# Kernel optimization log

Measured on AMD Instinct MI355X. Metric: run time of the kernel, lower is better.

The kernel has to match this reference:

```python
import jax, jax.numpy as jnp
import numpy as np

TAU = 1.5
K = 4
EPS = 1e-5
GN_GROUPS = 8

def conv2d(x, w, pad, rhs_dilation=(1, 1)):
    return jax.lax.conv_general_dilated(
        x, w, window_strides=(1, 1),
        padding=[(pad, pad), (pad, pad)],
        rhs_dilation=rhs_dilation,
        dimension_numbers=("NCHW", "OIHW", "NCHW"))

def setup_inputs() -> dict:
    key = jax.random.key(0)
    ks = jax.random.split(key, 16)
    s = 0.05  # weight scale to keep activations sane
    B, C, H, W = 16, 128, 64, 64
    O, HID, CG, SE = 128, 32, 16, 16
    d = {}
    d["x"] = jax.random.normal(ks[0], (B, C, H, W), jnp.float32)
    d["base_weight"] = jax.random.normal(ks[1], (O, C, 3, 3), jnp.float32) * s
    d["delta_weight"] = jax.random.normal(ks[2], (K, O, C, 3, 3), jnp.float32) * s
    d["kernel_scale"] = jnp.ones((K, O, 1, 1, 1), jnp.float32)
    d["gc_w1"] = jax.random.normal(ks[3], (HID, C), jnp.float32) * s
    d["gc_w2"] = jax.random.normal(ks[4], (C, HID), jnp.float32) * s
    d["rc_w"] = jax.random.normal(ks[5], (HID, C, 3, 3), jnp.float32) * s
    d["bn_gamma"] = jnp.ones((HID,), jnp.float32)
    d["bn_beta"] = jnp.zeros((HID,), jnp.float32)
    d["bn_mean"] = jnp.zeros((HID,), jnp.float32)
    d["bn_var"] = jnp.ones((HID,), jnp.float32)
    d["rg_w"] = jax.random.normal(ks[6], (HID, C), jnp.float32) * s
    d["gate_w"] = jax.random.normal(ks[7], (K * O, HID), jnp.float32) * s
    d["gate_b"] = jnp.zeros((K * O,), jnp.float32)
    d["cg_w1"] = jax.random.normal(ks[8], (CG, C), jnp.float32) * s
    d["cg_b1"] = jnp.zeros((CG,), jnp.float32)
    d["cg_w2"] = jax.random.normal(ks[9], (C, CG), jnp.float32) * s
    d["cg_b2"] = jnp.zeros((C,), jnp.float32)
    d["sg_w"] = jax.random.normal(ks[10], (1, 2, 7, 7), jnp.float32) * s
    d["gn_gamma"] = jnp.ones((O,), jnp.float32)
    d["gn_beta"] = jnp.zeros((O,), jnp.float32)
    d["se_w1"] = jax.random.normal(ks[11], (SE, O), jnp.float32) * s
    d["se_b1"] = jnp.zeros((SE,), jnp.float32)
    d["se_w2"] = jax.random.normal(ks[12], (O, SE), jnp.float32) * s
    d["se_b2"] = jnp.zeros((O,), jnp.float32)
    d["identity_scale"] = jnp.float32(0.0)
    d["bias"] = jnp.zeros((O,), jnp.float32)
    return d

def reference(x, base_weight, delta_weight, kernel_scale, gc_w1, gc_w2, rc_w,
              bn_gamma, bn_beta, bn_mean, bn_var, rg_w, gate_w, gate_b,
              cg_w1, cg_b1, cg_w2, cg_b2, sg_w, gn_gamma, gn_beta,
              se_w1, se_b1, se_w2, se_b2, identity_scale, bias):
    identity = x
    B, C, H, W = x.shape
    O = base_weight.shape[0]

    # global context gate (squeeze-excite style)
    p = x.mean((2, 3))                                    # [B,C]
    g = jax.nn.sigmoid(jax.nn.silu(p @ gc_w1.T) @ gc_w2.T)
    x = x * g[:, :, None, None]

    # channel gate
    pc = x.mean((2, 3))
    c_attn = jax.nn.sigmoid(jax.nn.silu(pc @ cg_w1.T + cg_b1) @ cg_w2.T + cg_b2)
    # spatial gate
    s_in = jnp.concatenate([x.mean(1, keepdims=True), x.max(1, keepdims=True)], axis=1)
    s_attn = jax.nn.sigmoid(conv2d(s_in, sg_w, pad=3))
    x = x * c_attn[:, :, None, None] * s_attn

    # router: dilated conv + BN(eval) + SiLU, plus global branch
    lf = conv2d(x, rc_w, pad=2, rhs_dilation=(2, 2))
    lf = (lf - bn_mean[None, :, None, None]) * jax.lax.rsqrt(bn_var + EPS)[None, :, None, None]
    lf = lf * bn_gamma[None, :, None, None] + bn_beta[None, :, None, None]
    lf = jax.nn.silu(lf)
    gf = jax.nn.silu(x.mean((2, 3)) @ rg_w.T)             # [B,HID]
    lf = lf + gf[:, :, None, None]
    alpha = jnp.einsum("bhij,oh->boij", lf, gate_w) + gate_b[None, :, None, None]
    alpha = alpha.reshape(B, K, O, H, W)
    alpha = jax.nn.softmax(alpha / TAU, axis=1)

    # unfold (k=3, stride=1, pad=1, dilation=1) -> H_out=H, W_out=W
    xp = jnp.pad(x, ((0, 0), (0, 0), (1, 1), (1, 1)))
    patches = jnp.stack([xp[:, :, i:i + H, j:j + W]
                         for i in range(3) for j in range(3)], axis=2)  # [B,C,9,H,W]
    L = H * W
    xu = patches.reshape(B, C * 9, L).transpose(0, 2, 1)  # [B,L,C*9]

    base = base_weight.reshape(O, -1)
    delta = (delta_weight * kernel_scale).reshape(K, O, -1)
    # same-size bilinear resize of alpha is the identity
    alpha_map = alpha.reshape(B, K, O, L)

    static = jnp.einsum("blf,of->bol", xu, base)          # [B,O,L]
    res = jnp.einsum("blf,kof->bkol", xu, delta)          # [B,K,O,L]
    final = static + (res * alpha_map).sum(1)
    out = final.reshape(B, O, H, W)

    # GroupNorm
    go = out.reshape(B, GN_GROUPS, O // GN_GROUPS, H, W)
    mu = go.mean((2, 3, 4), keepdims=True)
    var = go.var((2, 3, 4), keepdims=True)
    out = ((go - mu) * jax.lax.rsqrt(var + EPS)).reshape(B, O, H, W)
    out = out * gn_gamma[None, :, None, None] + gn_beta[None, :, None, None]

    # output SE
    ps = out.mean((2, 3))
    se = jax.nn.sigmoid(jax.nn.silu(ps @ se_w1.T + se_b1) @ se_w2.T + se_b2)
    out = out * se[:, :, None, None]

    out = out + jnp.tanh(identity_scale) * identity
    out = out + bias[None, :, None, None]
    return out
```

## Files before the change

kernel.cpp:

```cpp
#include <hip/hip_runtime.h>
#include <hip/hip_bf16.h>
#include <math.h>

typedef __bf16 bf16_t;
typedef __bf16 bf16x8 __attribute__((ext_vector_type(8)));
typedef __bf16 bf16x4 __attribute__((ext_vector_type(4)));
typedef float  f32x4  __attribute__((ext_vector_type(4)));

#define EPSF 1e-5f
#define TAUF 1.5f

__device__ __forceinline__ float sigmoidf_(float x){ return 1.f/(1.f+__expf(-x)); }
__device__ __forceinline__ float siluf_(float x){ return x*sigmoidf_(x); }

__device__ __forceinline__ void gload_lds16(const void* g, void* l){
  __builtin_amdgcn_global_load_lds((const __attribute__((address_space(1))) unsigned int*)g,
                                   (__attribute__((address_space(3))) unsigned int*)l, 16, 0, 0);
}

__global__ void k_prep(const float* __restrict__ base_w, const float* __restrict__ delta_w,
                       const float* __restrict__ kscale, const float* __restrict__ rc_w,
                       bf16_t* __restrict__ WCQ, bf16_t* __restrict__ RCWQ,
                       bf16_t* __restrict__ x2q,
                       const float* __restrict__ x, float* __restrict__ p){
  int bx = blockIdx.x;
  if (bx >= 2704){
    int bc = bx - 2704; const float* xr = x + (size_t)bc*4096;
    float s = 0.f;
    for (int i = threadIdx.x; i < 4096; i += 256) s += xr[i];
    __shared__ float sb[4];
    for (int off=32; off; off>>=1) s += __shfl_down(s, off);
    if ((threadIdx.x & 63)==0) sb[threadIdx.x>>6] = s;
    __syncthreads();
    if (threadIdx.x==0) p[bc] = (sb[0]+sb[1]+sb[2]+sb[3]) * (1.f/4096.f);
    return;
  }
  if (bx >= 2448){
    int pp = bx - 2448;
    size_t base = (size_t)pp*68*68*8;
    float4 z = {0.f,0.f,0.f,0.f};
    for (int i = threadIdx.x; i < 272; i += 256){
      int r = i/68; int wp = i - r*68;
      int hp = (r&1) + (r>>1)*66;
      *(float4*)(x2q + base + ((size_t)hp*68 + wp)*8) = z;
    }
    {
      int i = threadIdx.x;
      int hp = 2 + (i>>2);
      int wp = (i&1) + (i&2)*33;
      *(float4*)(x2q + base + ((size_t)hp*68 + wp)*8) = z;
    }
    return;
  }
  int i = bx*256 + threadIdx.x;
  if (i < 589824){
    int c8 = i&7; int o16 = (i>>3)&15; int q = (i>>7)&3; int s = (i>>9)&3;
    int h2 = (i>>11)&3; int r = i>>13; int t = r%9; int ob = r/9;
    int o = ob*16 + o16; int c = h2*32 + q*8 + c8;
    float v = base_w[(o*128+c)*9 + t] + delta_w[(((s*128)+o)*128 + c)*9 + t]*kscale[s*128+o];
    WCQ[i] = (bf16_t)v;
  } else if (i < 589824 + 36864){
    int j = i - 589824;
    int c8 = j&7; int h16 = (j>>3)&15; int q = (j>>7)&3; int n2 = (j>>9)&1;
    int r = j>>10; int t = r%9; int h2 = r/9;
    int hid = n2*16 + h16; int c = h2*32 + q*8 + c8;
    RCWQ[j] = (bf16_t)rc_w[(hid*128+c)*9 + t];
  }
}

__global__ void k_small1(const float* __restrict__ p, const float* __restrict__ gc_w1,
                         const float* __restrict__ gc_w2, const float* __restrict__ cg_w1,
                         const float* __restrict__ cg_b1, const float* __restrict__ cg_w2,
                         const float* __restrict__ cg_b2,
                         float* __restrict__ gbuf, float* __restrict__ gate){
  int b = blockIdx.x; int t = threadIdx.x;
  __shared__ float ps[128], h1[32], pc[128], c1[16];
  ps[t] = p[b*128+t];
  __syncthreads();
  if (t < 32){ float a=0.f; for(int c=0;c<128;c++) a += ps[c]*gc_w1[t*128+c]; h1[t]=siluf_(a); }
  __syncthreads();
  float a=0.f; for(int j=0;j<32;j++) a += h1[j]*gc_w2[t*32+j];
  float g = sigmoidf_(a);
  gbuf[b*128+t] = g; pc[t] = ps[t]*g;
  __syncthreads();
  if (t < 16){ float a2=cg_b1[t]; for(int c=0;c<128;c++) a2 += pc[c]*cg_w1[t*128+c]; c1[t]=siluf_(a2); }
  __syncthreads();
  float a3=cg_b2[t]; for(int j=0;j<16;j++) a3 += c1[j]*cg_w2[t*16+j];
  gate[b*128+t] = g * sigmoidf_(a3);
}

__global__ void k_spatial(const float* __restrict__ x, const float* __restrict__ gbuf,
                          float* __restrict__ sin_){
  int bi = blockIdx.x; int b = bi>>6; int h = bi&63;
  int wv = threadIdx.x>>6, w = threadIdx.x&63;
  __shared__ float psum[4][64], pmax[4][64];
  float sm=0.f, mx=-1e30f;
  const float* xb = x + (((size_t)b*128 + wv*32)*64 + h)*64 + w;
  const float* gb = gbuf + b*128 + wv*32;
  #pragma unroll 4
  for (int c=0;c<32;c++){
    float v = xb[(size_t)c*4096] * gb[c];
    sm += v; mx = fmaxf(mx, v);
  }
  psum[wv][w]=sm; pmax[wv][w]=mx;
  __syncthreads();
  if (threadIdx.x < 64){
    float s = psum[0][w]+psum[1][w]+psum[2][w]+psum[3][w];
    float m = fmaxf(fmaxf(pmax[0][w],pmax[1][w]),fmaxf(pmax[2][w],pmax[3][w]));
    sin_[b*8192 + h*64 + w]        = s*(1.f/128.f);
    sin_[b*8192 + 4096 + h*64 + w] = m;
  }
}

__global__ void __launch_bounds__(256) k_x2(
    const float* __restrict__ x, const float* __restrict__ gate,
    const float* __restrict__ sin_, const float* __restrict__ sg_w,
    bf16_t* __restrict__ x2q, float* __restrict__ pc2){
  int bi = blockIdx.x; int b = bi>>6; int h = bi&63;
  __shared__ float tile[128*65];
  __shared__ float sh_sin[980];
  __shared__ float sh_sgw[98];
  __shared__ float satt_row[64];
  int tid = threadIdx.x, wv = tid>>6, lane = tid&63;
  for (int i=tid;i<980;i+=256){
    int c2 = i/490; int rr = i - c2*490; int r = rr/70; int k = rr - r*70;
    int hh = h + r - 3; int ww = k - 3;
    float v = 0.f;
    if (hh>=0 && hh<64 && ww>=0 && ww<64) v = sin_[b*8192 + c2*4096 + hh*64 + ww];
    sh_sin[i] = v;
  }
  if (tid < 98) sh_sgw[tid] = sg_w[tid];
  __syncthreads();
  if (tid < 64){
    float a = 0.f;
    #pragma unroll
    for (int c2=0;c2<2;c2++)
      #pragma unroll
      for (int r=0;r<7;r++)
        #pragma unroll
        for (int j=0;j<7;j++)
          a += sh_sin[c2*490 + r*70 + tid + j] * sh_sgw[c2*49 + r*7 + j];
    satt_row[tid] = sigmoidf_(a);
  }
  __syncthreads();
  float sa = satt_row[lane];
  const float* xb = x + (((size_t)b*128 + wv*32)*64 + h)*64 + lane;
  const float* gb = gate + b*128 + wv*32;
  #pragma unroll 8
  for (int i=0;i<32;i++)
    tile[(wv*32+i)*65 + lane] = xb[(size_t)i*4096] * gb[i] * sa;
  __syncthreads();
  for (int it=0; it<4; it++){
    int idx = it*256 + tid;
    int cq = idx>>6; int w = idx&63;
    int c0 = cq*8;
    bf16x8 v;
    #pragma unroll
    for (int e=0;e<8;e++) v[e] = (bf16_t)tile[(c0+e)*65 + w];
    *(bf16x8*)(x2q + (((((size_t)b*4 + (cq>>2))*4 + (cq&3))*68 + (h+2))*68 + (w+2))*8) = v;
  }
  if (tid < 128){
    const float* row = &tile[tid*65];
    float s = 0.f;
    #pragma unroll 8
    for (int w=0;w<64;w++) s += row[w];
    atomicAdd(&pc2[b*128+tid], s);
  }
}

__global__ void __launch_bounds__(256) k_router(
    const bf16_t* __restrict__ x2q, const bf16_t* __restrict__ RCWQ,
    const float* __restrict__ bn_gamma, const float* __restrict__ bn_beta,
    const float* __restrict__ bn_mean, const float* __restrict__ bn_var,
    const float* __restrict__ pc2, const float* __restrict__ rg_w,
    bf16_t* __restrict__ lfb){
  __shared__ __align__(16) char smem[44544];
  __shared__ float sgf[32];
  __shared__ float spart[256];
  int tid = threadIdx.x;
  int wv = tid>>6, lane = tid&63, m16 = lane&15, q = lane>>4;
  int rb = blockIdx.x & 31, b = blockIdx.x >> 5;
  int r0 = rb*2;
  int rloc = wv&1;
  int ws0 = (wv>>1)*2;

  {
    int hid = tid&31, seg = tid>>5;
    float a=0.f;
    #pragma unroll
    for (int j=0;j<16;j++) a += pc2[b*128 + seg*16 + j]*rg_w[hid*128 + seg*16 + j];
    spart[tid] = a;
  }

  f32x4 acc[2][2] = {};

  #pragma unroll 1
  for (int h2=0; h2<4; h2++){
    const char* asrc = (const char*)(x2q + ((((size_t)(b*4+h2)*4 + wv)*68 + r0)*68)*8);
    #pragma unroll
    for (int j=0;j<7;j++){
      if (j*64 + lane < 408)
        gload_lds16(asrc + j*1024 + lane*16, (char*)smem + wv*6528 + j*1024);
    }
    const char* wsrc = (const char*)(RCWQ + (size_t)h2*9216) + wv*4608;
    #pragma unroll
    for (int j=0;j<5;j++){
      if (j*64 + lane < 288)
        gload_lds16(wsrc + j*1024 + lane*16, (char*)smem + 26112 + wv*4608 + j*1024);
    }
    __syncthreads();
    if (h2==0 && tid < 32){
      float s = 0.f;
      #pragma unroll
      for (int k=0;k<8;k++) s += spart[k*32+tid];
      sgf[tid] = siluf_(s*(1.f/4096.f));
    }
    #pragma unroll
    for (int t=0; t<9; t++){
      int di = t/3, dj = t - di*3;
      bf16x8 aw0 = *(const bf16x8*)((const char*)smem + 26112 + (t*2+0)*1024 + q*256 + m16*16);
      bf16x8 aw1 = *(const bf16x8*)((const char*)smem + 26112 + (t*2+1)*1024 + q*256 + m16*16);
      #pragma unroll
      for (int mt=0; mt<2; mt++){
        int wseg = ws0 + mt;
        bf16x8 bs = *(const bf16x8*)((const char*)smem + q*6528 +
                     ((rloc + 2*di)*68 + wseg*16 + m16 + 2*dj)*16);
        acc[0][mt] = __builtin_amdgcn_mfma_f32_16x16x32_bf16(aw0, bs, acc[0][mt], 0,0,0);
        acc[1][mt] = __builtin_amdgcn_mfma_f32_16x16x32_bf16(aw1, bs, acc[1][mt], 0,0,0);
      }
    }
    __syncthreads();
  }

  #pragma unroll
  for (int n2=0;n2<2;n2++){
    float aa[4], bb[4];
    #pragma unroll
    for (int i=0;i<4;i++){
      int hid = n2*16 + q*4 + i;
      float a = bn_gamma[hid]*rsqrtf(bn_var[hid]+EPSF);
      aa[i] = a;
      bb[i] = bn_beta[hid] - bn_mean[hid]*a;
    }
    #pragma unroll
    for (int mt=0;mt<2;mt++){
      bf16x4 yv;
      #pragma unroll
      for (int i=0;i<4;i++){
        int hid = n2*16 + q*4 + i;
        yv[i] = (bf16_t)(siluf_(aa[i]*acc[n2][mt][i] + bb[i]) + sgf[hid]);
      }
      size_t pos = (size_t)b*4096 + (r0+rloc)*64 + (ws0+mt)*16 + m16;
      *(bf16x4*)(lfb + pos*32 + n2*16 + q*4) = yv;
    }
  }
}

__global__ void __launch_bounds__(512, 2) k_main(
    const bf16_t* __restrict__ x2q, const bf16_t* __restrict__ WCQ,
    const bf16_t* __restrict__ lfb, const float* __restrict__ gate_w,
    const float* __restrict__ gate_b, bf16_t* __restrict__ outp,
    float* __restrict__ csum, float* __restrict__ cssq){
  __shared__ __align__(16) char smem[161920];
  float* sred = (float*)(smem + 160896);

  int tid = threadIdx.x;
  int wv = tid>>6, lane = tid&63, m16 = lane&15, q = lane>>4;
  int hf = wv>>2, w4 = wv&3;
  int bx = blockIdx.x;
  int ob2 = bx >> 7; int rem = bx & 127; int b = rem >> 3; int hb = rem & 7;
  int h0 = hb*8;
  int obase = (ob2*2 + hf)*16;

  auto STAGE_A = [&](int h2, int bsel){
    int quad = wv>>1, rh = wv&1;
    const char* asrc = (const char*)(x2q + ((((size_t)(b*4+h2)*4 + quad)*68 + (h0+1+rh*5))*68)*8);
    char* adst = (char*)smem + bsel*43584 + quad*10896 + rh*5440;
    #pragma unroll
    for (int j=0;j<6;j++){
      if (j*64 + lane < 340)
        gload_lds16(asrc + (j*64+lane)*16, adst + j*1024);
    }
  };
  auto STAGE_B = [&](int h2){
    int obh = ob2*2 + hf;
    const char* wsrc = (const char*)WCQ + (size_t)(obh*9*4 + h2)*4096;
    char* bdst = (char*)smem + 87168 + hf*36864 + w4*9216;
    #pragma unroll
    for (int j=0;j<9;j++){
      int cc = w4*576 + j*64 + lane;
      int tap = cc>>8, r = cc&255;
      gload_lds16(wsrc + tap*16384 + r*16, bdst + j*1024);
    }
  };

  f32x4 acc[8][4] = {};

  int baseA[8];
  #pragma unroll
  for (int mi=0;mi<8;mi++){
    int row = w4*2 + (mi>>2); int wseg = mi&3;
    baseA[mi] = q*10896 + (row*68 + wseg*16 + m16 + 1)*16;
  }
  int baseB = q*256 + m16*16;

  STAGE_A(0, 0);
  STAGE_B(0);

  #pragma unroll 1
  for (int h2=0; h2<4; h2++){
    if (h2 < 3){
      STAGE_A(h2+1, (h2+1)&1);
      asm volatile("s_waitcnt vmcnt(6)" ::: "memory");
    } else {
      asm volatile("s_waitcnt vmcnt(0)" ::: "memory");
    }
    __builtin_amdgcn_s_barrier();

    const char* Ab = (const char*)smem + (h2&1)*43584;
    const char* Bb = (const char*)smem + 87168 + hf*36864;
    #pragma unroll
    for (int t=0; t<9; t++){
      int di = t/3, dj = t - di*3;
      int toff = (di*68 + dj)*16;
      bf16x8 av[8], bv[4];
      #pragma unroll
      for (int mi=0;mi<8;mi++) av[mi] = *(const bf16x8*)(Ab + baseA[mi] + toff);
      #pragma unroll
      for (int s=0;s<4;s++)  bv[s] = *(const bf16x8*)(Bb + t*4096 + s*1024 + baseB);
      #pragma unroll
      for (int s=0;s<4;s++){
        #pragma unroll
        for (int mi=0;mi<8;mi++)
          acc[mi][s] = __builtin_amdgcn_mfma_f32_16x16x32_bf16(av[mi], bv[s], acc[mi][s], 0,0,0);
      }
    }
    __builtin_amdgcn_s_barrier();
    if (h2 < 3) STAGE_B(h2+1);
  }

  const char* lfsrc = (const char*)(lfb + ((size_t)b*4096 + h0*64)*32);
  #pragma unroll
  for (int j=0;j<4;j++)
    gload_lds16(lfsrc + j*8192 + wv*1024 + lane*16, (char*)smem + j*8192 + wv*1024);
  bf16_t* shGW = (bf16_t*)(smem + 32768);
  for (int idx = tid; idx < 4096; idx += 512){
    int hf2 = idx>>11; int n = (idx>>5)&63; int j2 = idx&31;
    shGW[idx] = (bf16_t)gate_w[((n>>4)*128 + (ob2*2+hf2)*16 + (n&15))*32 + j2];
  }
  __syncthreads();

  bf16x8 bg[4];
  #pragma unroll
  for (int kk=0;kk<4;kk++)
    bg[kk] = *(const bf16x8*)((const char*)shGW + hf*4096 + (kk*16+m16)*64 + q*16);
  float gb[4];
  #pragma unroll
  for (int kk=0;kk<4;kk++) gb[kk] = gate_b[kk*128 + obase + m16];

  const float itau = 1.f/TAUF;
  float s1 = 0.f, s2 = 0.f;
  size_t orow = ((size_t)(b*128 + obase + m16))*4096 + h0*64;
  #pragma unroll
  for (int mi=0; mi<8; mi++){
    bf16x8 avL = *(const bf16x8*)((const char*)smem + (w4*128 + mi*16 + m16)*64 + q*16);
    f32x4 zero = {};
    f32x4 lg[4];
    #pragma unroll
    for (int kk=0;kk<4;kk++)
      lg[kk] = __builtin_amdgcn_mfma_f32_16x16x32_bf16(avL, bg[kk], zero, 0,0,0);
    bf16x4 yv;
    #pragma unroll
    for (int r=0;r<4;r++){
      float l0 = (lg[0][r]+gb[0])*itau, l1 = (lg[1][r]+gb[1])*itau;
      float l2 = (lg[2][r]+gb[2])*itau, l3 = (lg[3][r]+gb[3])*itau;
      float mx = fmaxf(fmaxf(l0,l1),fmaxf(l2,l3));
      float e0=__expf(l0-mx), e1=__expf(l1-mx), e2=__expf(l2-mx), e3=__expf(l3-mx);
      float inv = 1.f/(e0+e1+e2+e3);
      float y = (e0*acc[mi][0][r] + e1*acc[mi][1][r]
               + e2*acc[mi][2][r] + e3*acc[mi][3][r])*inv;
      s1 += y; s2 += y*y;
      yv[r] = (bf16_t)y;
    }
    *(bf16x4*)(outp + orow + w4*128 + mi*16 + q*4) = yv;
  }

  s1 += __shfl_down(s1, 32); s1 += __shfl_down(s1, 16);
  s2 += __shfl_down(s2, 32); s2 += __shfl_down(s2, 16);
  if (lane < 16){ sred[wv*16 + lane] = s1; sred[128 + wv*16 + lane] = s2; }
  __syncthreads();
  if (tid < 32){
    int hf2 = tid>>4, o = tid&15;
    float a = 0.f, c = 0.f;
    #pragma unroll
    for (int k=0;k<4;k++){
      a += sred[(hf2*4+k)*16 + o];
      c += sred[128 + (hf2*4+k)*16 + o];
    }
    atomicAdd(&csum[b*128 + (ob2*2+hf2)*16 + o], a);
    atomicAdd(&cssq[b*128 + (ob2*2+hf2)*16 + o], c);
  }
}

__global__ void k_small3(const float* __restrict__ csum, const float* __restrict__ cssq,
                         const float* __restrict__ gn_gamma, const float* __restrict__ gn_beta,
                         const float* __restrict__ se_w1, const float* __restrict__ se_b1,
                         const float* __restrict__ se_w2, const float* __restrict__ se_b2,
                         float* __restrict__ sca, float* __restrict__ shb){
  int b = blockIdx.x; int o = threadIdx.x;
  __shared__ float s1[128], s2[128], gmu[8], grs[8], psl[128], t1[16];
  s1[o] = csum[b*128+o]; s2[o] = cssq[b*128+o];
  __syncthreads();
  if (o<8){
    float a=0.f,a2=0.f; for(int j=0;j<16;j++){ a+=s1[o*16+j]; a2+=s2[o*16+j]; }
    float mu = a*(1.f/65536.f); float var = a2*(1.f/65536.f) - mu*mu;
    gmu[o]=mu; grs[o]=rsqrtf(var+EPSF);
  }
  __syncthreads();
  int g = o>>4;
  psl[o] = (s1[o]*(1.f/4096.f) - gmu[g])*grs[g]*gn_gamma[o] + gn_beta[o];
  __syncthreads();
  if (o<16){ float a = se_b1[o]; for(int c=0;c<128;c++) a += psl[c]*se_w1[o*128+c]; t1[o]=siluf_(a); }
  __syncthreads();
  float a = se_b2[o]; for(int j=0;j<16;j++) a += t1[j]*se_w2[o*16+j];
  float sev = sigmoidf_(a);
  sca[b*128+o] = grs[g]*gn_gamma[o]*sev;
  shb[b*128+o] = (gn_beta[o] - gmu[g]*grs[g]*gn_gamma[o])*sev;
}

__global__ void k_final(const bf16_t* __restrict__ outp, const float* __restrict__ x,
                        const float* __restrict__ sca, const float* __restrict__ shb,
                        const float* __restrict__ bias, const float* __restrict__ iscale,
                        float* __restrict__ out){
  float ts = tanhf(iscale[0]);
  size_t i = ((size_t)blockIdx.x*256 + threadIdx.x)*8;
  int bo = (int)(i>>12); int o = bo&127;
  float A = sca[bo], Bv = shb[bo] + bias[o];
  bf16x8 ov = *(const bf16x8*)(outp + i);
  float4 x0 = *(const float4*)(x+i), x1 = *(const float4*)(x+i+4);
  float4 r0, r1;
  r0.x = (float)ov[0]*A + Bv + ts*x0.x;
  r0.y = (float)ov[1]*A + Bv + ts*x0.y;
  r0.z = (float)ov[2]*A + Bv + ts*x0.z;
  r0.w = (float)ov[3]*A + Bv + ts*x0.w;
  r1.x = (float)ov[4]*A + Bv + ts*x1.x;
  r1.y = (float)ov[5]*A + Bv + ts*x1.y;
  r1.z = (float)ov[6]*A + Bv + ts*x1.z;
  r1.w = (float)ov[7]*A + Bv + ts*x1.w;
  *(float4*)(out+i) = r0; *(float4*)(out+i+4) = r1;
}

extern "C" void kernel_launch(void* const* d_in, const int* in_sizes, int n_in,
                              void* d_out, int out_size, void* d_ws, size_t ws_size,
                              hipStream_t stream){
  const float* x      = (const float*)d_in[0];
  const float* base_w = (const float*)d_in[1];
  const float* delta_w= (const float*)d_in[2];
  const float* kscale = (const float*)d_in[3];
  const float* gc_w1  = (const float*)d_in[4];
  const float* gc_w2  = (const float*)d_in[5];
  const float* rc_w   = (const float*)d_in[6];
  const float* bn_g   = (const float*)d_in[7];
  const float* bn_b   = (const float*)d_in[8];
  const float* bn_m   = (const float*)d_in[9];
  const float* bn_v   = (const float*)d_in[10];
  const float* rg_w   = (const float*)d_in[11];
  const float* gate_w = (const float*)d_in[12];
  const float* gate_b = (const float*)d_in[13];
  const float* cg_w1  = (const float*)d_in[14];
  const float* cg_b1  = (const float*)d_in[15];
  const float* cg_w2  = (const float*)d_in[16];
  const float* cg_b2  = (const float*)d_in[17];
  const float* sg_w   = (const float*)d_in[18];
  const float* gn_g   = (const float*)d_in[19];
  const float* gn_b   = (const float*)d_in[20];
  const float* se_w1  = (const float*)d_in[21];
  const float* se_b1  = (const float*)d_in[22];
  const float* se_w2  = (const float*)d_in[23];
  const float* se_b2  = (const float*)d_in[24];
  const float* iscale = (const float*)d_in[25];
  const float* bias   = (const float*)d_in[26];
  float* out = (float*)d_out;

  char* ws = (char*)d_ws;
  size_t off = 0;
  auto alloc = [&](size_t bytes)->void*{ void* p = ws + off; off += (bytes + 255) & ~(size_t)255; return p; };
  bf16_t* X2Q = (bf16_t*)alloc(16ull*4*4*68*68*8*2);
  bf16_t* WCQ = (bf16_t*)alloc(589824ull*2);
  bf16_t* RCWQ= (bf16_t*)alloc(36864ull*2);
  bf16_t* LF  = (bf16_t*)alloc(16ull*4096*32*2);
  bf16_t* OUTP= (bf16_t*)alloc(16ull*128*4096*2);
  float* PC2  = (float*)alloc(2048*4);
  float* CSUM = (float*)alloc(2048*4);
  float* CSSQ = (float*)alloc(2048*4);
  float* P    = (float*)alloc(2048*4);
  float* GB   = (float*)alloc(2048*4);
  float* GATE = (float*)alloc(2048*4);
  float* SIN  = (float*)alloc(16ull*8192*4);
  float* SCA  = (float*)alloc(2048*4);
  float* SHB  = (float*)alloc(2048*4);

  (void)hipMemsetAsync(PC2, 0, 3*8192, stream);

  k_prep   <<<4752, 256, 0, stream>>>(base_w, delta_w, kscale, rc_w, WCQ, RCWQ, X2Q, x, P);
  k_small1 <<<16,   128, 0, stream>>>(P, gc_w1, gc_w2, cg_w1, cg_b1, cg_w2, cg_b2, GB, GATE);
  k_spatial<<<1024, 256, 0, stream>>>(x, GB, SIN);
  k_x2     <<<1024, 256, 0, stream>>>(x, GATE, SIN, sg_w, X2Q, PC2);
  k_router <<<512,  256, 0, stream>>>(X2Q, RCWQ, bn_g, bn_b, bn_m, bn_v, PC2, rg_w, LF);
  k_main   <<<512,  512, 0, stream>>>(X2Q, WCQ, LF, gate_w, gate_b, OUTP, CSUM, CSSQ);
  k_small3 <<<16,   128, 0, stream>>>(CSUM, CSSQ, gn_g, gn_b, se_w1, se_b1, se_w2, se_b2, SCA, SHB);
  k_final  <<<4096, 256, 0, stream>>>(OUTP, x, SCA, SHB, bias, iscale, out);
}
```

Before: 258.5 us.

## Fold tiny gating and SE kernels into consumers and drop memset launch

New measurement: 266.9 us. 3.3% more time.

```diff
diff --git a/kernel.cpp b/kernel.cpp
--- a/kernel.cpp
+++ b/kernel.cpp
@@ -22,8 +22,15 @@
                        const float* __restrict__ kscale, const float* __restrict__ rc_w,
                        bf16_t* __restrict__ WCQ, bf16_t* __restrict__ RCWQ,
                        bf16_t* __restrict__ x2q,
-                       const float* __restrict__ x, float* __restrict__ p){
+                       const float* __restrict__ x, float* __restrict__ p,
+                       float* __restrict__ zbase){
   int bx = blockIdx.x;
+  if (bx >= 4752){
+    float4 z = {0.f,0.f,0.f,0.f};
+    for (int i = threadIdx.x; i < 1536; i += 256)
+      *(float4*)(zbase + i*4) = z;
+    return;
+  }
   if (bx >= 2704){
     int bc = bx - 2704; const float* xr = x + (size_t)bc*4096;
     float s = 0.f;
@@ -68,43 +75,29 @@
   }
 }
 
-__global__ void k_small1(const float* __restrict__ p, const float* __restrict__ gc_w1,
-                         const float* __restrict__ gc_w2, const float* __restrict__ cg_w1,
-                         const float* __restrict__ cg_b1, const float* __restrict__ cg_w2,
-                         const float* __restrict__ cg_b2,
-                         float* __restrict__ gbuf, float* __restrict__ gate){
-  int b = blockIdx.x; int t = threadIdx.x;
-  __shared__ float ps[128], h1[32], pc[128], c1[16];
-  ps[t] = p[b*128+t];
-  __syncthreads();
-  if (t < 32){ float a=0.f; for(int c=0;c<128;c++) a += ps[c]*gc_w1[t*128+c]; h1[t]=siluf_(a); }
-  __syncthreads();
-  float a=0.f; for(int j=0;j<32;j++) a += h1[j]*gc_w2[t*32+j];
-  float g = sigmoidf_(a);
-  gbuf[b*128+t] = g; pc[t] = ps[t]*g;
-  __syncthreads();
-  if (t < 16){ float a2=cg_b1[t]; for(int c=0;c<128;c++) a2 += pc[c]*cg_w1[t*128+c]; c1[t]=siluf_(a2); }
-  __syncthreads();
-  float a3=cg_b2[t]; for(int j=0;j<16;j++) a3 += c1[j]*cg_w2[t*16+j];
-  gate[b*128+t] = g * sigmoidf_(a3);
-}
-
-__global__ void k_spatial(const float* __restrict__ x, const float* __restrict__ gbuf,
+__global__ void k_spatial(const float* __restrict__ x, const float* __restrict__ p,
+                          const float* __restrict__ gc_w1, const float* __restrict__ gc_w2,
                           float* __restrict__ sin_){
   int bi = blockIdx.x; int b = bi>>6; int h = bi&63;
-  int wv = threadIdx.x>>6, w = threadIdx.x&63;
+  int tid = threadIdx.x, wv = tid>>6, w = tid&63;
   __shared__ float psum[4][64], pmax[4][64];
+  __shared__ float ps[128], h1[32], gsh[128];
+  if (tid < 128) ps[tid] = p[b*128+tid];
+  __syncthreads();
+  if (tid < 32){ float a=0.f; for(int c=0;c<128;c++) a += ps[c]*gc_w1[tid*128+c]; h1[tid]=siluf_(a); }
+  __syncthreads();
+  if (tid < 128){ float a=0.f; for(int j=0;j<32;j++) a += h1[j]*gc_w2[tid*32+j]; gsh[tid]=sigmoidf_(a); }
+  __syncthreads();
   float sm=0.f, mx=-1e30f;
   const float* xb = x + (((size_t)b*128 + wv*32)*64 + h)*64 + w;
-  const float* gb = gbuf + b*128 + wv*32;
   #pragma unroll 4
   for (int c=0;c<32;c++){
-    float v = xb[(size_t)c*4096] * gb[c];
+    float v = xb[(size_t)c*4096] * gsh[wv*32+c];
     sm += v; mx = fmaxf(mx, v);
   }
   psum[wv][w]=sm; pmax[wv][w]=mx;
   __syncthreads();
-  if (threadIdx.x < 64){
+  if (tid < 64){
     float s = psum[0][w]+psum[1][w]+psum[2][w]+psum[3][w];
     float m = fmaxf(fmaxf(pmax[0][w],pmax[1][w]),fmaxf(pmax[2][w],pmax[3][w]));
     sin_[b*8192 + h*64 + w]        = s*(1.f/128.f);
@@ -113,7 +106,10 @@
 }
 
 __global__ void __launch_bounds__(256) k_x2(
-    const float* __restrict__ x, const float* __restrict__ gate,
+    const float* __restrict__ x, const float* __restrict__ p,
+    const float* __restrict__ gc_w1, const float* __restrict__ gc_w2,
+    const float* __restrict__ cg_w1, const float* __restrict__ cg_b1,
+    const float* __restrict__ cg_w2, const float* __restrict__ cg_b2,
     const float* __restrict__ sin_, const float* __restrict__ sg_w,
     bf16_t* __restrict__ x2q, float* __restrict__ pc2){
   int bi = blockIdx.x; int b = bi>>6; int h = bi&63;
@@ -121,6 +117,7 @@
   __shared__ float sh_sin[980];
   __shared__ float sh_sgw[98];
   __shared__ float satt_row[64];
+  __shared__ float ps[128], h1[32], gsh[128], pcs[128], c1[16], gate_sh[128];
   int tid = threadIdx.x, wv = tid>>6, lane = tid&63;
   for (int i=tid;i<980;i+=256){
     int c2 = i/490; int rr = i - c2*490; int r = rr/70; int k = rr - r*70;
@@ -130,8 +127,12 @@
     sh_sin[i] = v;
   }
   if (tid < 98) sh_sgw[tid] = sg_w[tid];
-  __syncthreads();
-  if (tid < 64){
+  if (tid < 128) ps[tid] = p[b*128+tid];
+  __syncthreads();
+  if (tid < 32){
+    float a=0.f; for(int c=0;c<128;c++) a += ps[c]*gc_w1[tid*128+c]; h1[tid]=siluf_(a);
+  } else if (tid >= 128 && tid < 192){
+    int col = tid - 128;
     float a = 0.f;
     #pragma unroll
     for (int c2=0;c2<2;c2++)
@@ -139,16 +140,30 @@
       for (int r=0;r<7;r++)
         #pragma unroll
         for (int j=0;j<7;j++)
-          a += sh_sin[c2*490 + r*70 + tid + j] * sh_sgw[c2*49 + r*7 + j];
-    satt_row[tid] = sigmoidf_(a);
+          a += sh_sin[c2*490 + r*70 + col + j] * sh_sgw[c2*49 + r*7 + j];
+    satt_row[col] = sigmoidf_(a);
+  }
+  __syncthreads();
+  if (tid < 128){
+    float a=0.f; for(int j=0;j<32;j++) a += h1[j]*gc_w2[tid*32+j];
+    float g = sigmoidf_(a);
+    gsh[tid] = g; pcs[tid] = ps[tid]*g;
+  }
+  __syncthreads();
+  if (tid < 16){
+    float a2=cg_b1[tid]; for(int c=0;c<128;c++) a2 += pcs[c]*cg_w1[tid*128+c]; c1[tid]=siluf_(a2);
+  }
+  __syncthreads();
+  if (tid < 128){
+    float a3=cg_b2[tid]; for(int j=0;j<16;j++) a3 += c1[j]*cg_w2[tid*16+j];
+    gate_sh[tid] = gsh[tid]*sigmoidf_(a3);
   }
   __syncthreads();
   float sa = satt_row[lane];
   const float* xb = x + (((size_t)b*128 + wv*32)*64 + h)*64 + lane;
-  const float* gb = gate + b*128 + wv*32;
   #pragma unroll 8
   for (int i=0;i<32;i++)
-    tile[(wv*32+i)*65 + lane] = xb[(size_t)i*4096] * gb[i] * sa;
+    tile[(wv*32+i)*65 + lane] = xb[(size_t)i*4096] * gate_sh[wv*32+i] * sa;
   __syncthreads();
   for (int it=0; it<4; it++){
     int idx = it*256 + tid;
@@ -402,52 +417,58 @@
   }
 }
 
-__global__ void k_small3(const float* __restrict__ csum, const float* __restrict__ cssq,
-                         const float* __restrict__ gn_gamma, const float* __restrict__ gn_beta,
-                         const float* __restrict__ se_w1, const float* __restrict__ se_b1,
-                         const float* __restrict__ se_w2, const float* __restrict__ se_b2,
-                         float* __restrict__ sca, float* __restrict__ shb){
-  int b = blockIdx.x; int o = threadIdx.x;
-  __shared__ float s1[128], s2[128], gmu[8], grs[8], psl[128], t1[16];
-  s1[o] = csum[b*128+o]; s2[o] = cssq[b*128+o];
-  __syncthreads();
-  if (o<8){
-    float a=0.f,a2=0.f; for(int j=0;j<16;j++){ a+=s1[o*16+j]; a2+=s2[o*16+j]; }
+__global__ void __launch_bounds__(256) k_final(
+    const bf16_t* __restrict__ outp, const float* __restrict__ x,
+    const float* __restrict__ csum, const float* __restrict__ cssq,
+    const float* __restrict__ gn_gamma, const float* __restrict__ gn_beta,
+    const float* __restrict__ se_w1, const float* __restrict__ se_b1,
+    const float* __restrict__ se_w2, const float* __restrict__ se_b2,
+    const float* __restrict__ bias, const float* __restrict__ iscale,
+    float* __restrict__ out){
+  int bo = blockIdx.x; int b = bo>>7; int o = bo&127;
+  int tid = threadIdx.x;
+  __shared__ float s1[128], s2[128], gmu[8], grs[8], psl[128], t1[16], scb[2];
+  if (tid < 128){ s1[tid] = csum[b*128+tid]; s2[tid] = cssq[b*128+tid]; }
+  __syncthreads();
+  if (tid < 8){
+    float a=0.f,a2=0.f; for(int j=0;j<16;j++){ a+=s1[tid*16+j]; a2+=s2[tid*16+j]; }
     float mu = a*(1.f/65536.f); float var = a2*(1.f/65536.f) - mu*mu;
-    gmu[o]=mu; grs[o]=rsqrtf(var+EPSF);
-  }
-  __syncthreads();
-  int g = o>>4;
-  psl[o] = (s1[o]*(1.f/4096.f) - gmu[g])*grs[g]*gn_gamma[o] + gn_beta[o];
-  __syncthreads();
-  if (o<16){ float a = se_b1[o]; for(int c=0;c<128;c++) a += psl[c]*se_w1[o*128+c]; t1[o]=siluf_(a); }
-  __syncthreads();
-  float a = se_b2[o]; for(int j=0;j<16;j++) a += t1[j]*se_w2[o*16+j];
-  float sev = sigmoidf_(a);
-  sca[b*128+o] = grs[g]*gn_gamma[o]*sev;
-  shb[b*128+o] = (gn_beta[o] - gmu[g]*grs[g]*gn_gamma[o])*sev;
-}
-
-__global__ void k_final(const bf16_t* __restrict__ outp, const float* __restrict__ x,
-                        const float* __restrict__ sca, const float* __restrict__ shb,
-                        const float* __restrict__ bias, const float* __restrict__ iscale,
-                        float* __restrict__ out){
+    gmu[tid]=mu; grs[tid]=rsqrtf(var+EPSF);
+  }
+  __syncthreads();
+  if (tid < 128){
+    int g = tid>>4;
+    psl[tid] = (s1[tid]*(1.f/4096.f) - gmu[g])*grs[g]*gn_gamma[tid] + gn_beta[tid];
+  }
+  __syncthreads();
+  if (tid < 16){ float a = se_b1[tid]; for(int c=0;c<128;c++) a += psl[c]*se_w1[tid*128+c]; t1[tid]=siluf_(a); }
+  __syncthreads();
+  if (tid == 0){
+    float a = se_b2[o]; for(int j=0;j<16;j++) a += t1[j]*se_w2[o*16+j];
+    float sev = sigmoidf_(a); int g = o>>4;
+    scb[0] = grs[g]*gn_gamma[o]*sev;
+    scb[1] = (gn_beta[o] - gmu[g]*grs[g]*gn_gamma[o])*sev;
+  }
+  __syncthreads();
   float ts = tanhf(iscale[0]);
-  size_t i = ((size_t)blockIdx.x*256 + threadIdx.x)*8;
-  int bo = (int)(i>>12); int o = bo&127;
-  float A = sca[bo], Bv = shb[bo] + bias[o];
-  bf16x8 ov = *(const bf16x8*)(outp + i);
-  float4 x0 = *(const float4*)(x+i), x1 = *(const float4*)(x+i+4);
-  float4 r0, r1;
-  r0.x = (float)ov[0]*A + Bv + ts*x0.x;
-  r0.y = (float)ov[1]*A + Bv + ts*x0.y;
-  r0.z = (float)ov[2]*A + Bv + ts*x0.z;
-  r0.w = (float)ov[3]*A + Bv + ts*x0.w;
-  r1.x = (float)ov[4]*A + Bv + ts*x1.x;
-  r1.y = (float)ov[5]*A + Bv + ts*x1.y;
-  r1.z = (float)ov[6]*A + Bv + ts*x1.z;
-  r1.w = (float)ov[7]*A + Bv + ts*x1.w;
-  *(float4*)(out+i) = r0; *(float4*)(out+i+4) = r1;
+  float A = scb[0], Bv = scb[1] + bias[o];
+  size_t base = (size_t)bo*4096 + tid*16;
+  #pragma unroll
+  for (int hh=0; hh<2; hh++){
+    size_t i = base + hh*8;
+    bf16x8 ov = *(const bf16x8*)(outp + i);
+    float4 x0 = *(const float4*)(x+i), x1 = *(const float4*)(x+i+4);
+    float4 r0, r1;
+    r0.x = (float)ov[0]*A + Bv + ts*x0.x;
+    r0.y = (float)ov[1]*A + Bv + ts*x0.y;
+    r0.z = (float)ov[2]*A + Bv + ts*x0.z;
+    r0.w = (float)ov[3]*A + Bv + ts*x0.w;
+    r1.x = (float)ov[4]*A + Bv + ts*x1.x;
+    r1.y = (float)ov[5]*A + Bv + ts*x1.y;
+    r1.z = (float)ov[6]*A + Bv + ts*x1.z;
+    r1.w = (float)ov[7]*A + Bv + ts*x1.w;
+    *(float4*)(out+i) = r0; *(float4*)(out+i+4) = r1;
+  }
 }
 
 extern "C" void kernel_launch(void* const* d_in, const int* in_sizes, int n_in,
@@ -494,20 +515,12 @@
   float* CSUM = (float*)alloc(2048*4);
   float* CSSQ = (float*)alloc(2048*4);
   float* P    = (float*)alloc(2048*4);
-  float* GB   = (float*)alloc(2048*4);
-  float* GATE = (float*)alloc(2048*4);
   float* SIN  = (float*)alloc(16ull*8192*4);
-  float* SCA  = (float*)alloc(2048*4);
-  float* SHB  = (float*)alloc(2048*4);
-
-  (void)hipMemsetAsync(PC2, 0, 3*8192, stream);
-
-  k_prep   <<<4752, 256, 0, stream>>>(base_w, delta_w, kscale, rc_w, WCQ, RCWQ, X2Q, x, P);
-  k_small1 <<<16,   128, 0, stream>>>(P, gc_w1, gc_w2, cg_w1, cg_b1, cg_w2, cg_b2, GB, GATE);
-  k_spatial<<<1024, 256, 0, stream>>>(x, GB, SIN);
-  k_x2     <<<1024, 256, 0, stream>>>(x, GATE, SIN, sg_w, X2Q, PC2);
+
+  k_prep   <<<4753, 256, 0, stream>>>(base_w, delta_w, kscale, rc_w, WCQ, RCWQ, X2Q, x, P, PC2);
+  k_spatial<<<1024, 256, 0, stream>>>(x, P, gc_w1, gc_w2, SIN);
+  k_x2     <<<1024, 256, 0, stream>>>(x, P, gc_w1, gc_w2, cg_w1, cg_b1, cg_w2, cg_b2, SIN, sg_w, X2Q, PC2);
   k_router <<<512,  256, 0, stream>>>(X2Q, RCWQ, bn_g, bn_b, bn_m, bn_v, PC2, rg_w, LF);
   k_main   <<<512,  512, 0, stream>>>(X2Q, WCQ, LF, gate_w, gate_b, OUTP, CSUM, CSSQ);
-  k_small3 <<<16,   128, 0, stream>>>(CSUM, CSSQ, gn_g, gn_b, se_w1, se_b1, se_w2, se_b2, SCA, SHB);
-  k_final  <<<4096, 256, 0, stream>>>(OUTP, x, SCA, SHB, bias, iscale, out);
-}
+  k_final  <<<2048, 256, 0, stream>>>(OUTP, x, CSUM, CSSQ, gn_g, gn_b, se_w1, se_b1, se_w2, se_b2, bias, iscale, out);
+}
```
